# Performance work log

Measured on AMD Instinct MI355X. Metric: run time of the kernel, lower is better.

Reference implementation:

```python
import jax, jax.numpy as jnp
import numpy as np

HIDDEN_DIM = 768
N_HEAD = 12
ATTN_DIM = HIDDEN_DIM // N_HEAD  # 64
SCALE = jnp.sqrt(jnp.float32(ATTN_DIM))


def setup_inputs() -> dict:
    key = jax.random.key(0)
    ks = jax.random.split(key, 6)
    B, S = 8, 2048
    return {
        "query": jax.random.normal(ks[0], (B, S, HIDDEN_DIM), dtype=jnp.float32),
        "key": jax.random.normal(ks[1], (B, S, HIDDEN_DIM), dtype=jnp.float32),
        "value": jax.random.normal(ks[2], (B, S, HIDDEN_DIM), dtype=jnp.float32),
        "Wq": jax.random.normal(ks[3], (ATTN_DIM, HIDDEN_DIM), dtype=jnp.float32) * 0.02,
        "Wk": jax.random.normal(ks[4], (ATTN_DIM, HIDDEN_DIM), dtype=jnp.float32) * 0.02,
        "Wv": jax.random.normal(ks[5], (ATTN_DIM, HIDDEN_DIM), dtype=jnp.float32) * 0.02,
    }


def reference(query, key, value, Wq, Wk, Wv):
    # Linear projections (bias=False): x @ W.T -> [B, S, attn_dim]
    q = jnp.einsum("bsh,dh->bsd", query, Wq)
    k = jnp.einsum("bsh,dh->bsd", key, Wk)
    v = jnp.einsum("bsh,dh->bsd", value, Wv)
    # Scaled dot-product scores: [B, S, S]
    scores = jnp.einsum("bqd,bkd->bqk", q, k) / SCALE
    attn = jax.nn.softmax(scores, axis=-1)  # dropout p=0 -> identity in eval
    # Weighted sum of values: [B, S, attn_dim]
    return jnp.einsum("bqk,bkd->bqd", attn, v)
```

## Files before the change

kernel.cpp:

```cpp
#include <hip/hip_runtime.h>
#include <hip/hip_bf16.h>

typedef short s16x8 __attribute__((ext_vector_type(8)));
typedef float f32x4 __attribute__((ext_vector_type(4)));
typedef unsigned short us4 __attribute__((ext_vector_type(4)));

static __device__ __forceinline__ unsigned short f2bf(float f) {
  unsigned u = __builtin_bit_cast(unsigned, f);
  u += 0x7FFFu + ((u >> 16) & 1u);
  return (unsigned short)(u >> 16);
}

static __device__ __forceinline__ unsigned pk2(float a, float b) {
  __hip_bfloat162 h = __float22bfloat162_rn(make_float2(a, b));
  unsigned r;
  __builtin_memcpy(&r, &h, 4);
  return r;
}

#if __has_builtin(__builtin_amdgcn_exp2f)
#define EXP2(x) __builtin_amdgcn_exp2f(x)
#else
#define EXP2(x) exp2f(x)
#endif

#define QSCALE 0.1803368801111204f

#define MFMA16(a, b, c) __builtin_amdgcn_mfma_f32_16x16x32_bf16((a), (b), (c), 0, 0, 0)

__global__ __launch_bounds__(256) void proj_kernel(
    const float* __restrict__ Xq, const float* __restrict__ Xk, const float* __restrict__ Xv,
    const float* __restrict__ Wq, const float* __restrict__ Wk, const float* __restrict__ Wv,
    unsigned short* __restrict__ qf,
    unsigned short* __restrict__ kf,
    unsigned short* __restrict__ vfo)
{
  __shared__ __align__(16) unsigned short xs[64][72];
  __shared__ __align__(16) unsigned short ws[64][72];

  const int bid = blockIdx.x;
  const int t = bid >> 8;
  const int rb = bid & 255;
  const int b = rb >> 5;
  const int stile = rb & 31;
  const float* X = (t == 0) ? Xq : (t == 1) ? Xk : Xv;
  const float* W = (t == 0) ? Wq : (t == 1) ? Wk : Wv;

  const int tid = threadIdx.x;
  const int wv = tid >> 6;
  const int lane = tid & 63;
  const int j = lane & 15;
  const int g = lane >> 4;

  f32x4 acc[4];
#pragma unroll
  for (int i = 0; i < 4; ++i) acc[i] = {0.f, 0.f, 0.f, 0.f};

  const size_t xrow0 = (size_t)b * 2048 + (size_t)stile * 64;

  for (int kc = 0; kc < 768; kc += 64) {
#pragma unroll
    for (int p = 0; p < 4; ++p) {
      int lin = p * 256 + tid;
      int row = lin >> 4;
      int seg = lin & 15;
      float4 xv = *(const float4*)(X + (xrow0 + row) * 768 + kc + seg * 4);
      uint2 ux; ux.x = pk2(xv.x, xv.y); ux.y = pk2(xv.z, xv.w);
      *(uint2*)&xs[row][seg * 4] = ux;
      float4 wv4 = *(const float4*)(W + (size_t)row * 768 + kc + seg * 4);
      uint2 uw; uw.x = pk2(wv4.x, wv4.y); uw.y = pk2(wv4.z, wv4.w);
      *(uint2*)&ws[row][seg * 4] = uw;
    }
    __syncthreads();
    s16x8 a0 = *(const s16x8*)&xs[wv * 16 + j][g * 8];
    s16x8 a1 = *(const s16x8*)&xs[wv * 16 + j][32 + g * 8];
#pragma unroll
    for (int ct = 0; ct < 4; ++ct) {
      s16x8 b0 = *(const s16x8*)&ws[ct * 16 + j][g * 8];
      s16x8 b1 = *(const s16x8*)&ws[ct * 16 + j][32 + g * 8];
      acc[ct] = MFMA16(a0, b0, acc[ct]);
      acc[ct] = MFMA16(a1, b1, acc[ct]);
    }
    __syncthreads();
  }

  unsigned short* fb = &xs[0][0];
  if (t < 2) {
    const float sc = (t == 0) ? QSCALE : 1.0f;
#pragma unroll
    for (int ct = 0; ct < 4; ++ct) {
      int base16 = wv * 1024 + ((ct >= 2) ? 512 : 0) + (((ct & 1) * 2 + (j >> 3)) * 128) + (j & 7);
#pragma unroll
      for (int r = 0; r < 4; ++r)
        fb[base16 + (g * 4 + r) * 8] = f2bf(acc[ct][r] * sc);
    }
    __syncthreads();
    unsigned short* dst = ((t == 0) ? qf : kf) + ((size_t)b * 128 + stile * 4) * 1024;
#pragma unroll
    for (int p2 = 0; p2 < 2; ++p2) {
      int idx = p2 * 2048 + tid * 8;
      *(s16x8*)(dst + idx) = *(const s16x8*)&fb[idx];
    }
  } else {
#pragma unroll
    for (int ct = 0; ct < 4; ++ct) {
      uint2 uv; uv.x = pk2(acc[ct][0], acc[ct][1]); uv.y = pk2(acc[ct][2], acc[ct][3]);
      *(uint2*)&fb[ct * 1024 + ((wv >= 2) ? 512 : 0) +
                   (((wv & 1) * 2 + (g >> 1)) * 16 + j) * 8 + (g & 1) * 4] = uv;
    }
    __syncthreads();
    unsigned short* gb = vfo + ((size_t)b * 32 + stile) * 4096;
#pragma unroll
    for (int p2 = 0; p2 < 2; ++p2) {
      int idx = p2 * 2048 + tid * 8;
      *(s16x8*)(gb + idx) = *(const s16x8*)&fb[idx];
    }
  }
}

__global__ __launch_bounds__(512, 4) void attn_kernel(
    const unsigned short* __restrict__ qf,
    const unsigned short* __restrict__ kf,
    const unsigned short* __restrict__ vf,
    float* __restrict__ out)
{
  __shared__ __align__(16) unsigned char raw[69632];
  __shared__ float lls[8][32];
  unsigned short* p_lds = (unsigned short*)raw;
  float* comb = (float*)raw;

  const int tid = threadIdx.x;
  const int wv = tid >> 6;
  const int lane = tid & 63;
  const int j = lane & 15;
  const int g = lane >> 4;

  const int bid0 = blockIdx.x;
  const int swz = (bid0 & 7) * 64 + (bid0 >> 3);
  const int b = swz >> 6;
  const int qt = swz & 63;

  s16x8 q0[2], q1[2];
#pragma unroll
  for (int rg = 0; rg < 2; ++rg) {
    const unsigned short* qp =
        qf + ((size_t)(b * 128 + qt * 2 + rg)) * 1024 + lane * 8;
    q0[rg] = *(const s16x8*)(qp);
    q1[rg] = *(const s16x8*)(qp + 512);
  }

  f32x4 o[2][4];
#pragma unroll
  for (int rg = 0; rg < 2; ++rg)
#pragma unroll
    for (int i = 0; i < 4; ++i) o[rg][i] = {0.f, 0.f, 0.f, 0.f};
  float l_acc[2] = {0.f, 0.f};

  const unsigned short* kfb = kf + (size_t)b * 131072 + wv * 16384 + lane * 8;
  const unsigned short* vfb = vf + (size_t)b * 131072 + wv * 16384 + lane * 8;
  unsigned short* myp0 = p_lds + (size_t)((wv * 2 + 0) * 16 + j) * 72;
  unsigned short* myp1 = p_lds + (size_t)((wv * 2 + 1) * 16 + j) * 72;

  for (int kt = 0; kt < 4; ++kt) {
    const unsigned short* kc_ = kfb + kt * 4096;
    s16x8 ka[4], kb2[4];
#pragma unroll
    for (int ct = 0; ct < 4; ++ct) {
      ka[ct] = *(const s16x8*)(kc_ + ct * 1024);
      kb2[ct] = *(const s16x8*)(kc_ + ct * 1024 + 512);
    }
    {
      f32x4 st[4];
#pragma unroll
      for (int ct = 0; ct < 4; ++ct) {
        f32x4 z = {0.f, 0.f, 0.f, 0.f};
        z = MFMA16(ka[ct], q0[0], z);
        z = MFMA16(kb2[ct], q1[0], z);
        st[ct] = z;
      }
#pragma unroll
      for (int ct = 0; ct < 4; ++ct) {
        float p0 = EXP2(st[ct][0]);
        float p1 = EXP2(st[ct][1]);
        float p2 = EXP2(st[ct][2]);
        float p3 = EXP2(st[ct][3]);
        l_acc[0] += (p0 + p1) + (p2 + p3);
        uint2 u; u.x = pk2(p0, p1); u.y = pk2(p2, p3);
        *(uint2*)&myp0[ct * 16 + g * 4] = u;
      }
    }
    {
      f32x4 st[4];
#pragma unroll
      for (int ct = 0; ct < 4; ++ct) {
        f32x4 z = {0.f, 0.f, 0.f, 0.f};
        z = MFMA16(ka[ct], q0[1], z);
        z = MFMA16(kb2[ct], q1[1], z);
        st[ct] = z;
      }
#pragma unroll
      for (int ct = 0; ct < 4; ++ct) {
        float p0 = EXP2(st[ct][0]);
        float p1 = EXP2(st[ct][1]);
        float p2 = EXP2(st[ct][2]);
        float p3 = EXP2(st[ct][3]);
        l_acc[1] += (p0 + p1) + (p2 + p3);
        uint2 u; u.x = pk2(p0, p1); u.y = pk2(p2, p3);
        *(uint2*)&myp1[ct * 16 + g * 4] = u;
      }
    }
    const unsigned short* vc_ = vfb + kt * 4096;
    s16x8 va[4], vb2[4];
#pragma unroll
    for (int dt = 0; dt < 4; ++dt) {
      va[dt] = *(const s16x8*)(vc_ + dt * 1024);
      vb2[dt] = *(const s16x8*)(vc_ + dt * 1024 + 512);
    }
    s16x8 pa0 = *(const s16x8*)&myp0[g * 8];
    s16x8 pa1 = *(const s16x8*)&myp0[32 + g * 8];
#pragma unroll
    for (int dt = 0; dt < 4; ++dt) {
      o[0][dt] = MFMA16(pa0, va[dt], o[0][dt]);
      o[0][dt] = MFMA16(pa1, vb2[dt], o[0][dt]);
    }
    s16x8 pb0 = *(const s16x8*)&myp1[g * 8];
    s16x8 pb1 = *(const s16x8*)&myp1[32 + g * 8];
#pragma unroll
    for (int dt = 0; dt < 4; ++dt) {
      o[1][dt] = MFMA16(pb0, va[dt], o[1][dt]);
      o[1][dt] = MFMA16(pb1, vb2[dt], o[1][dt]);
    }
  }

#pragma unroll
  for (int rg = 0; rg < 2; ++rg) {
    l_acc[rg] += __shfl_xor(l_acc[rg], 16);
    l_acc[rg] += __shfl_xor(l_acc[rg], 32);
  }

  __syncthreads();
#pragma unroll
  for (int rg = 0; rg < 2; ++rg) {
#pragma unroll
    for (int dt = 0; dt < 4; ++dt)
#pragma unroll
      for (int r = 0; r < 4; ++r)
        comb[((size_t)wv * 32 + rg * 16 + g * 4 + r) * 68 + dt * 16 + j] = o[rg][dt][r];
    if (g == 0) lls[wv][rg * 16 + j] = l_acc[rg];
  }
  __syncthreads();

#pragma unroll
  for (int it = 0; it < 4; ++it) {
    const int idx = it * 512 + tid;
    const int row = idx >> 6;
    const int d = idx & 63;
    float s = 0.f, lt = 0.f;
#pragma unroll
    for (int cc = 0; cc < 8; ++cc) {
      s += comb[((size_t)cc * 32 + row) * 68 + d];
      lt += lls[cc][row];
    }
    out[(((size_t)b * 2048) + qt * 32 + row) * 64 + d] = s / lt;
  }
}

extern "C" void kernel_launch(void* const* d_in, const int* in_sizes, int n_in,
                              void* d_out, int out_size, void* d_ws, size_t ws_size,
                              hipStream_t stream) {
  const float* query = (const float*)d_in[0];
  const float* key_  = (const float*)d_in[1];
  const float* value = (const float*)d_in[2];
  const float* Wq = (const float*)d_in[3];
  const float* Wk = (const float*)d_in[4];
  const float* Wv = (const float*)d_in[5];

  unsigned short* qfb = (unsigned short*)d_ws;
  unsigned short* kfb = qfb + 1048576u;
  unsigned short* vfb = qfb + 2u * 1048576u;
  float* outp = (float*)d_out;

  hipLaunchKernelGGL(proj_kernel, dim3(768), dim3(256), 0, stream,
                     query, key_, value, Wq, Wk, Wv, qfb, kfb, vfb);
  hipLaunchKernelGGL(attn_kernel, dim3(512), dim3(512), 0, stream,
                     qfb, kfb, vfb, outp);
}
```

Before: 45.36 us.

## Halve LDS combine buffer and stream K/V loads to raise occupancy

The cross-wave output combine is split into two halves, so the shared buffer shrinks to about half its size. Launch bounds rise from 4 to 6 blocks per SM. K and V fragments are now loaded per column tile inside the MFMA loops rather than all up front, which cuts register pressure. The aim is more resident waves to hide global-load latency, at the cost of less load batching and an extra barrier in the epilogue.

```diff
diff --git a/kernel.cpp b/kernel.cpp
--- a/kernel.cpp
+++ b/kernel.cpp
@@ -118,13 +118,13 @@
   }
 }
 
-__global__ __launch_bounds__(512, 4) void attn_kernel(
+__global__ __launch_bounds__(512, 6) void attn_kernel(
     const unsigned short* __restrict__ qf,
     const unsigned short* __restrict__ kf,
     const unsigned short* __restrict__ vf,
     float* __restrict__ out)
 {
-  __shared__ __align__(16) unsigned char raw[69632];
+  __shared__ __align__(16) unsigned char raw[36864];
   __shared__ float lls[8][32];
   unsigned short* p_lds = (unsigned short*)raw;
   float* comb = (float*)raw;
@@ -163,72 +163,42 @@
 
   for (int kt = 0; kt < 4; ++kt) {
     const unsigned short* kc_ = kfb + kt * 4096;
-    s16x8 ka[4], kb2[4];
-#pragma unroll
-    for (int ct = 0; ct < 4; ++ct) {
-      ka[ct] = *(const s16x8*)(kc_ + ct * 1024);
-      kb2[ct] = *(const s16x8*)(kc_ + ct * 1024 + 512);
-    }
-    {
-      f32x4 st[4];
-#pragma unroll
-      for (int ct = 0; ct < 4; ++ct) {
-        f32x4 z = {0.f, 0.f, 0.f, 0.f};
-        z = MFMA16(ka[ct], q0[0], z);
-        z = MFMA16(kb2[ct], q1[0], z);
-        st[ct] = z;
-      }
-#pragma unroll
-      for (int ct = 0; ct < 4; ++ct) {
-        float p0 = EXP2(st[ct][0]);
-        float p1 = EXP2(st[ct][1]);
-        float p2 = EXP2(st[ct][2]);
-        float p3 = EXP2(st[ct][3]);
+#pragma unroll
+    for (int ct = 0; ct < 4; ++ct) {
+      s16x8 ka = *(const s16x8*)(kc_ + ct * 1024);
+      s16x8 kb2 = *(const s16x8*)(kc_ + ct * 1024 + 512);
+      f32x4 z0 = {0.f, 0.f, 0.f, 0.f};
+      z0 = MFMA16(ka, q0[0], z0);
+      z0 = MFMA16(kb2, q1[0], z0);
+      f32x4 z1 = {0.f, 0.f, 0.f, 0.f};
+      z1 = MFMA16(ka, q0[1], z1);
+      z1 = MFMA16(kb2, q1[1], z1);
+      {
+        float p0 = EXP2(z0[0]), p1 = EXP2(z0[1]), p2 = EXP2(z0[2]), p3 = EXP2(z0[3]);
         l_acc[0] += (p0 + p1) + (p2 + p3);
         uint2 u; u.x = pk2(p0, p1); u.y = pk2(p2, p3);
         *(uint2*)&myp0[ct * 16 + g * 4] = u;
       }
-    }
-    {
-      f32x4 st[4];
-#pragma unroll
-      for (int ct = 0; ct < 4; ++ct) {
-        f32x4 z = {0.f, 0.f, 0.f, 0.f};
-        z = MFMA16(ka[ct], q0[1], z);
-        z = MFMA16(kb2[ct], q1[1], z);
-        st[ct] = z;
-      }
-#pragma unroll
-      for (int ct = 0; ct < 4; ++ct) {
-        float p0 = EXP2(st[ct][0]);
-        float p1 = EXP2(st[ct][1]);
-        float p2 = EXP2(st[ct][2]);
-        float p3 = EXP2(st[ct][3]);
+      {
+        float p0 = EXP2(z1[0]), p1 = EXP2(z1[1]), p2 = EXP2(z1[2]), p3 = EXP2(z1[3]);
         l_acc[1] += (p0 + p1) + (p2 + p3);
         uint2 u; u.x = pk2(p0, p1); u.y = pk2(p2, p3);
         *(uint2*)&myp1[ct * 16 + g * 4] = u;
       }
     }
     const unsigned short* vc_ = vfb + kt * 4096;
-    s16x8 va[4], vb2[4];
-#pragma unroll
-    for (int dt = 0; dt < 4; ++dt) {
-      va[dt] = *(const s16x8*)(vc_ + dt * 1024);
-      vb2[dt] = *(const s16x8*)(vc_ + dt * 1024 + 512);
-    }
     s16x8 pa0 = *(const s16x8*)&myp0[g * 8];
     s16x8 pa1 = *(const s16x8*)&myp0[32 + g * 8];
-#pragma unroll
-    for (int dt = 0; dt < 4; ++dt) {
-      o[0][dt] = MFMA16(pa0, va[dt], o[0][dt]);
-      o[0][dt] = MFMA16(pa1, vb2[dt], o[0][dt]);
-    }
     s16x8 pb0 = *(const s16x8*)&myp1[g * 8];
     s16x8 pb1 = *(const s16x8*)&myp1[32 + g * 8];
 #pragma unroll
     for (int dt = 0; dt < 4; ++dt) {
-      o[1][dt] = MFMA16(pb0, va[dt], o[1][dt]);
-      o[1][dt] = MFMA16(pb1, vb2[dt], o[1][dt]);
+      s16x8 va = *(const s16x8*)(vc_ + dt * 1024);
+      s16x8 vb2 = *(const s16x8*)(vc_ + dt * 1024 + 512);
+      o[0][dt] = MFMA16(pa0, va, o[0][dt]);
+      o[0][dt] = MFMA16(pa1, vb2, o[0][dt]);
+      o[1][dt] = MFMA16(pb0, va, o[1][dt]);
+      o[1][dt] = MFMA16(pb1, vb2, o[1][dt]);
     }
   }
 
@@ -236,32 +206,32 @@
   for (int rg = 0; rg < 2; ++rg) {
     l_acc[rg] += __shfl_xor(l_acc[rg], 16);
     l_acc[rg] += __shfl_xor(l_acc[rg], 32);
-  }
-
+    if (g == 0) lls[wv][rg * 16 + j] = l_acc[rg];
+  }
   __syncthreads();
-#pragma unroll
-  for (int rg = 0; rg < 2; ++rg) {
+
+#pragma unroll
+  for (int half = 0; half < 2; ++half) {
 #pragma unroll
     for (int dt = 0; dt < 4; ++dt)
 #pragma unroll
       for (int r = 0; r < 4; ++r)
-        comb[((size_t)wv * 32 + rg * 16 + g * 4 + r) * 68 + dt * 16 + j] = o[rg][dt][r];
-    if (g == 0) lls[wv][rg * 16 + j] = l_acc[rg];
-  }
-  __syncthreads();
-
-#pragma unroll
-  for (int it = 0; it < 4; ++it) {
-    const int idx = it * 512 + tid;
-    const int row = idx >> 6;
-    const int d = idx & 63;
-    float s = 0.f, lt = 0.f;
-#pragma unroll
-    for (int cc = 0; cc < 8; ++cc) {
-      s += comb[((size_t)cc * 32 + row) * 68 + d];
-      lt += lls[cc][row];
-    }
-    out[(((size_t)b * 2048) + qt * 32 + row) * 64 + d] = s / lt;
+        comb[((size_t)wv * 16 + g * 4 + r) * 68 + dt * 16 + j] = o[half][dt][r];
+    __syncthreads();
+#pragma unroll
+    for (int it = 0; it < 2; ++it) {
+      const int idx = it * 512 + tid;
+      const int row = idx >> 6;
+      const int d = idx & 63;
+      float s = 0.f, lt = 0.f;
+#pragma unroll
+      for (int cc = 0; cc < 8; ++cc) {
+        s += comb[((size_t)cc * 16 + row) * 68 + d];
+        lt += lls[cc][half * 16 + row];
+      }
+      out[(((size_t)b * 2048) + qt * 32 + half * 16 + row) * 64 + d] = s / lt;
+    }
+    __syncthreads();
   }
 }
 
```

Measured after the change: 79.05 us. 1.74x slower.
